# Optimization experiments

Measured on AMD Instinct MI355X. Metric: run time of the kernel, lower is better.

The kernel has to match this reference:

```python
import jax, jax.numpy as jnp
import numpy as np

B, N, H, NH, E = 4, 512, 1024, 16, 8
DH = H // NH  # head dim 64


def setup_inputs() -> dict:
    key = jax.random.key(0)
    ks = jax.random.split(key, 8)
    return {
        "hidden_states": jax.random.normal(ks[0], (B, N, H), jnp.float32),
        "attn_mask": jax.random.randint(ks[1], (N, N), 0, 2, jnp.int32),
        "key_padding_mask": jax.random.randint(ks[2], (B, N), 0, 2, jnp.int32),
        "w_gate": jax.random.normal(ks[3], (H, E), jnp.float32) * 0.02,
        "w_qkv": jax.random.normal(ks[4], (E, H, 3 * H), jnp.float32) * 0.02,
        "b_qkv": jnp.zeros((E, 3 * H), jnp.float32),
        "w_dense": jax.random.normal(ks[5], (E, H, H), jnp.float32) * 0.02,
        "b_dense": jnp.zeros((E, H), jnp.float32),
    }


def _moe_apply(x, combine, w, b):
    # x: [T,H], combine: [T,E] (one-hot * gate prob), w: [E,H,D], b: [E,D]
    out_all = jnp.einsum('th,ehd->etd', x, w) + b[:, None, :]  # [E,T,D]
    return jnp.einsum('te,etd->td', combine, out_all)


def reference(hidden_states, attn_mask, key_padding_mask, w_gate, w_qkv, b_qkv, w_dense, b_dense):
    b, n, h = hidden_states.shape
    # attention_mask = logical_or(attn_mask[None], key_padding_mask[:,None]) -> [B,N,N], then [:,None]*-1e4
    mask = jnp.logical_or(attn_mask[None].astype(bool), key_padding_mask[:, None].astype(bool))
    mask_bias = mask[:, None, :, :].astype(hidden_states.dtype) * (-10000.0)  # [B,1,N,N]

    x = hidden_states.reshape(-1, h)  # [T,H]
    gate = jax.nn.softmax(x @ w_gate, axis=-1)  # [T,E]
    # top-1 routing; combine weight = gate prob of chosen expert
    idx = jnp.argmax(gate, axis=-1)
    combine = jax.nn.one_hot(idx, gate.shape[-1], dtype=gate.dtype) * jnp.max(gate, axis=-1, keepdims=True)

    qkv = _moe_apply(x, combine, w_qkv, b_qkv).reshape(b, n, 3 * h)
    q, k, v = jnp.split(qkv, 3, axis=-1)
    # transpose_for_scores: [B,N,H] -> [B,NH,N,DH]
    to_heads = lambda t: t.reshape(b, n, NH, DH).transpose(0, 2, 1, 3)
    q, k, v = to_heads(q), to_heads(k), to_heads(v)

    scores = jnp.einsum('bhqd,bhkd->bhqk', q, k) / (float(DH) ** 0.5) + mask_bias
    attn_probs = jax.nn.softmax(scores, axis=-1)  # dropout p=0 -> identity
    ctx = jnp.einsum('bhqk,bhkd->bhqd', attn_probs, v)
    ctx = ctx.transpose(0, 2, 1, 3).reshape(-1, h)  # [T,H]

    out = _moe_apply(ctx, combine, w_dense, b_dense).reshape(b, n, h)
    return out, attn_probs
```

## Files before the change

### kernel.cpp

```cpp
#include <hip/hip_runtime.h>


typedef short short8 __attribute__((ext_vector_type(8)));
typedef float f32x4 __attribute__((ext_vector_type(4)));

constexpr int Bsz  = 4;
constexpr int Nseq = 512;
constexpr int Hdim = 1024;
constexpr int NHd  = 16;
constexpr int Ex   = 8;
constexpr int DHd  = 64;
constexpr int T    = Bsz * Nseq;
constexpr int H3   = 3 * Hdim;
constexpr int MAXT128 = 24;
constexpr int KB_N = 32;
constexpr int NPH  = KB_N / 2;

__device__ inline unsigned short f2bf(float f) {
  union { float f; unsigned u; } v{f};
  unsigned r = v.u + 0x7fffu + ((v.u >> 16) & 1u);
  return (unsigned short)(r >> 16);
}
__device__ inline float bf2f(unsigned short s) {
  union { unsigned u; float f; } v{(unsigned)s << 16};
  return v.f;
}
__device__ inline unsigned cvtpk2(float lo, float hi) {
  unsigned r;
  asm("v_cvt_pk_bf16_f32 %0, %1, %2" : "=v"(r) : "v"(lo), "v"(hi));
  return r;
}
__device__ inline void gl16(const unsigned short* g, unsigned short* l) {
  __builtin_amdgcn_global_load_lds(
      (const __attribute__((address_space(1))) unsigned int*)(g),
      (__attribute__((address_space(3))) unsigned int*)(l), 16, 0, 0);
}

__global__ __launch_bounds__(64) void gate_kernel(
    const float* __restrict__ x, const float* __restrict__ wg,
    float* __restrict__ prob, int* __restrict__ expert,
    unsigned short* __restrict__ Xb) {
  int t = blockIdx.x;
  int l = threadIdx.x;
  const float* xr = x + (size_t)t * Hdim;
  float acc[Ex] = {0, 0, 0, 0, 0, 0, 0, 0};
  for (int h = l; h < Hdim; h += 64) {
    float xv = xr[h];
    const float4* wr = (const float4*)(wg + (size_t)h * Ex);
    float4 w0 = wr[0], w1 = wr[1];
    acc[0] += xv * w0.x; acc[1] += xv * w0.y; acc[2] += xv * w0.z; acc[3] += xv * w0.w;
    acc[4] += xv * w1.x; acc[5] += xv * w1.y; acc[6] += xv * w1.z; acc[7] += xv * w1.w;
  }
  {
    const float4* s = (const float4*)(xr + l * 16);
    float4 f0 = s[0], f1 = s[1], f2 = s[2], f3 = s[3];
    unsigned q[8] = {cvtpk2(f0.x, f0.y), cvtpk2(f0.z, f0.w),
                     cvtpk2(f1.x, f1.y), cvtpk2(f1.z, f1.w),
                     cvtpk2(f2.x, f2.y), cvtpk2(f2.z, f2.w),
                     cvtpk2(f3.x, f3.y), cvtpk2(f3.z, f3.w)};
    uint4* d = (uint4*)(Xb + (size_t)t * Hdim + l * 16);
    d[0] = *(uint4*)&q[0];
    d[1] = *(uint4*)&q[4];
  }
#pragma unroll
  for (int e = 0; e < Ex; e++) {
#pragma unroll
    for (int off = 32; off > 0; off >>= 1) acc[e] += __shfl_down(acc[e], off);
  }
  if (l == 0) {
    float m = acc[0]; int mi = 0;
#pragma unroll
    for (int e = 1; e < Ex; e++) if (acc[e] > m) { m = acc[e]; mi = e; }
    float s = 0.f;
#pragma unroll
    for (int e = 0; e < Ex; e++) s += expf(acc[e] - m);
    prob[t]   = 1.0f / s;
    expert[t] = mi;
  }
}

__global__ __launch_bounds__(256) void prep_kernel(
    const float* __restrict__ Wq, const float* __restrict__ Wd,
    unsigned short* __restrict__ WtQ, unsigned short* __restrict__ WtD,
    const int* __restrict__ expert, int* offs, int* meta, int* te, int* tr,
    int* __restrict__ perm) {
  int bx = blockIdx.x, kb2 = blockIdx.y, e = blockIdx.z;
  int tid = threadIdx.x;

  if (bx == 32) {
    if (kb2 != 0 || e != 0) return;
    __shared__ int cnt[Ex];
    __shared__ int cur[Ex];
    if (tid < Ex) cnt[tid] = 0;
    __syncthreads();
    for (int t = tid; t < T; t += 256) atomicAdd(&cnt[expert[t]], 1);
    __syncthreads();
    if (tid == 0) {
      int o = 0, nt = 0;
      for (int ee = 0; ee < Ex; ee++) {
        offs[ee] = o; cur[ee] = o;
        int c = cnt[ee];
        for (int r = 0; r < c; r += 128) { te[nt] = ee; tr[nt] = o + r; nt++; }
        o += c;
      }
      offs[Ex] = o;
      meta[0] = nt;
    }
    __syncthreads();
    for (int t = tid; t < T; t += 256) {
      int slot = atomicAdd(&cur[expert[t]], 1);
      perm[slot] = t;
    }
    return;
  }

  const float* W;
  unsigned short* Wt;
  int ncb, NCOLS, NCB;
  if (bx < 24) { W = Wq; Wt = WtQ; ncb = bx;      NCOLS = H3;   NCB = 24; }
  else         { W = Wd; Wt = WtD; ncb = bx - 24; NCOLS = Hdim; NCB = 8;  }

  int c4 = tid & 31;
  int kg = (tid >> 5) & 3;
  int kh = tid >> 7;
  int kb = kb2 * 2 + kh;

  const float* src = W + ((size_t)e * Hdim + kb * 32 + kg * 8) * NCOLS + ncb * 128 + c4 * 4;
  float4 f[8];
#pragma unroll
  for (int j = 0; j < 8; j++) f[j] = *(const float4*)(src + (size_t)j * NCOLS);

  unsigned short* dst = Wt + (((size_t)e * NCB + ncb) * KB_N + kb) * 4096 +
                        (size_t)((c4 >> 2) * 64 + kg * 16 + (c4 & 3) * 4) * 8;
#pragma unroll
  for (int i = 0; i < 4; i++) {
    unsigned q[4] = {cvtpk2(f[0][i], f[1][i]), cvtpk2(f[2][i], f[3][i]),
                     cvtpk2(f[4][i], f[5][i]), cvtpk2(f[6][i], f[7][i])};
    *(uint4*)(dst + (size_t)i * 8) = *(uint4*)q;
  }
}

template <int BN>
__global__ __launch_bounds__(256) void moe_gemm_v13(
    const unsigned short* __restrict__ Xb, const unsigned short* __restrict__ Wt,
    const float* __restrict__ bias, const float* __restrict__ prob,
    const int* __restrict__ perm, const int* __restrict__ offs,
    const int* __restrict__ metap, const int* __restrict__ tile_e,
    const int* __restrict__ tile_r,
    unsigned short* __restrict__ Ybf, float* __restrict__ Yf, int Ncols) {
  constexpr int NF = BN / 32;
  int tIdx = blockIdx.y;
  if (tIdx >= metap[0]) return;
  int e = tile_e[tIdx], row0 = tile_r[tIdx];
  int rows = offs[e + 1] - row0; if (rows > 128) rows = 128;
  int col0 = blockIdx.x * BN;
  int ncb_n = Ncols >> 7;

  __shared__ unsigned short As[2 * 8192];
  __shared__ int   tok_s[128];
  __shared__ float p_s[128];

  int tid = threadIdx.x;
  if (tid < 128) {
    int rr = tid < rows ? tid : rows - 1;
    int tok = perm[row0 + rr];
    tok_s[tid] = tok; p_s[tid] = prob[tok];
  }
  __syncthreads();

  int lane = tid & 63, wave = tid >> 6;
  int l15 = lane & 15, l4 = lane >> 4;
  int wr = wave >> 1, wc = wave & 1;
  int aslotr = l4 ^ ((l15 >> 1) & 3);

  int arow0 = wave * 16 + (lane >> 2);
  int arow1 = arow0 + 64;
  int aslot0 = (lane & 3) ^ ((arow0 >> 1) & 3);
  int aslot1 = (lane & 3) ^ ((arow1 >> 1) & 3);
  const unsigned short* ag0 = Xb + (size_t)tok_s[arow0] * Hdim + aslot0 * 8;
  const unsigned short* ag1 = Xb + (size_t)tok_s[arow1] * Hdim + aslot1 * 8;

  const unsigned short* btile = Wt + (((size_t)e * ncb_n + (col0 >> 7)) * KB_N) * 4096;
  int Fb = ((col0 & 127) >> 4) + wc * NF;
  const unsigned short* bfrag = btile + ((size_t)(Fb * 64 + lane)) * 8;

  f32x4 acc[4][NF] = {};
  short8 bq[2][2][NF];

  gl16(ag0 + 0 * 32, As + 0 + wave * 512);
  gl16(ag1 + 0 * 32, As + 2048 + wave * 512);
  gl16(ag0 + 1 * 32, As + 4096 + wave * 512);
  gl16(ag1 + 1 * 32, As + 4096 + 2048 + wave * 512);
  asm volatile("" ::: "memory");
#pragma unroll
  for (int t = 0; t < 2; t++)
#pragma unroll
    for (int n = 0; n < NF; n++)
      bq[0][t][n] = *(const short8*)(bfrag + (size_t)t * 4096 + n * 512);
#pragma unroll
  for (int t = 0; t < 2; t++)
#pragma unroll
    for (int n = 0; n < NF; n++)
      bq[1][t][n] = *(const short8*)(bfrag + (size_t)(2 + t) * 4096 + n * 512);
  asm volatile("" ::: "memory");

#define PHASE(PH, PAR)                                                             \
  {                                                                                \
    int kap = ((PH) + 1 < NPH) ? (PH) + 1 : NPH - 1;      \
    int kbp = ((PH) + 2 < NPH) ? (PH) + 2 : NPH - 1;      \
    asm volatile("s_waitcnt vmcnt(4) lgkmcnt(0)" ::: "memory");                    \
    __builtin_amdgcn_s_barrier();                                                  \
    asm volatile("" ::: "memory");                                                 \
    unsigned short* dA = As + ((PAR) ^ 1) * 8192;                                  \
    gl16(ag0 + (size_t)(2 * kap) * 32, dA + wave * 512);                           \
    gl16(ag1 + (size_t)(2 * kap) * 32, dA + 2048 + wave * 512);                    \
    gl16(ag0 + (size_t)(2 * kap + 1) * 32, dA + 4096 + wave * 512);                \
    gl16(ag1 + (size_t)(2 * kap + 1) * 32, dA + 4096 + 2048 + wave * 512);         \
    asm volatile("" ::: "memory");                                                 \
    _Pragma("unroll")                                                              \
    for (int t = 0; t < 2; t++) {                                                  \
      const unsigned short* rb = As + (PAR) * 8192 + t * 4096;                     \
      short8 a[4];                                                                 \
      _Pragma("unroll")                                                            \
      for (int m = 0; m < 4; m++)                                                  \
        a[m] = *(const short8*)&rb[(wr * 64 + m * 16 + l15) * 32 + aslotr * 8];    \
      _Pragma("unroll")                                                            \
      for (int n = 0; n < NF; n++)                                                 \
        _Pragma("unroll")                                                          \
        for (int m = 0; m < 4; m++)                                                \
          acc[m][n] = __builtin_amdgcn_mfma_f32_16x16x32_bf16(                     \
              a[m], bq[PAR][t][n], acc[m][n], 0, 0, 0);                            \
    }                                                                              \
    _Pragma("unroll")                                                              \
    for (int t = 0; t < 2; t++)                                                    \
      _Pragma("unroll")                                                            \
      for (int n = 0; n < NF; n++)                                                 \
        bq[PAR][t][n] =                                                            \
            *(const short8*)(bfrag + (size_t)(2 * kbp + t) * 4096 + n * 512);      \
  }

  for (int ph = 0; ph < NPH; ph += 2) {
    PHASE(ph, 0);
    PHASE(ph + 1, 1);
  }
#undef PHASE
  asm volatile("s_waitcnt vmcnt(0)" ::: "memory");

#pragma unroll
  for (int n = 0; n < NF; n++) {
    int colg = col0 + wc * (NF * 16) + n * 16 + l15;
    float bv = bias[(size_t)e * Ncols + colg];
#pragma unroll
    for (int m = 0; m < 4; m++) {
#pragma unroll
      for (int r = 0; r < 4; r++) {
        int row = wr * 64 + m * 16 + l4 * 4 + r;
        if (row < rows) {
          int tok = tok_s[row];
          float o = (acc[m][n][r] + bv) * p_s[row];
          if (Ybf) Ybf[(size_t)tok * Ncols + colg] = f2bf(o);
          else     Yf [(size_t)tok * Ncols + colg] = o;
        }
      }
    }
  }
}

__global__ __launch_bounds__(256) void attn_kernel(
    const unsigned short* __restrict__ qkvb, const int* __restrict__ attn_mask,
    const int* __restrict__ kp_mask, float* __restrict__ probs_out,
    unsigned short* __restrict__ ctxb) {
  int qt = blockIdx.x, h = blockIdx.y, b = blockIdx.z;
  int tid = threadIdx.x;

  __shared__ unsigned short Qs[32 * 72];
  __shared__ unsigned short KV[2][64 * 72];
  __shared__ unsigned short S[32 * 520];
  __shared__ float invs[32];

  int lane = tid & 63, wave = tid >> 6;
  int l15 = lane & 15, l4 = lane >> 4;

  {
    int r = tid >> 3, c = (tid & 7) * 8;
    int t = b * Nseq + qt * 32 + r;
    uint4 v = *(const uint4*)(qkvb + (size_t)t * H3 + h * DHd + c);
    unsigned short* u = (unsigned short*)&v;
    unsigned short tmp[8];
#pragma unroll
    for (int j = 0; j < 8; j++) tmp[j] = f2bf(bf2f(u[j]) * 0.125f);
    *(uint4*)&Qs[r * 72 + c] = *(uint4*)tmp;
  }

  int kr0 = tid >> 3, kc0 = (tid & 7) * 8;
  int kr1 = kr0 + 32;
  const unsigned short* kbase = qkvb + (size_t)(b * Nseq) * H3 + Hdim + h * DHd + kc0;
  uint4 rc0 = *(const uint4*)(kbase + (size_t)kr0 * H3);
  uint4 rc1 = *(const uint4*)(kbase + (size_t)kr1 * H3);
  int cur = 0;
  for (int kt = 0; kt < 8; kt++) {
    int kn = (kt + 1 < 8) ? kt + 1 : 7;
    uint4 nn0 = *(const uint4*)(kbase + (size_t)(kn * 64 + kr0) * H3);
    uint4 nn1 = *(const uint4*)(kbase + (size_t)(kn * 64 + kr1) * H3);
    *(uint4*)&KV[cur][kr0 * 72 + kc0] = rc0;
    *(uint4*)&KV[cur][kr1 * 72 + kc0] = rc1;
    asm volatile("s_waitcnt lgkmcnt(0)" ::: "memory");
    __builtin_amdgcn_s_barrier();
    asm volatile("" ::: "memory");

    f32x4 acc[2] = {};
#pragma unroll
    for (int kk = 0; kk < 2; kk++) {
      short8 bfr = *(const short8*)&KV[cur][(wave * 16 + l15) * 72 + kk * 32 + l4 * 8];
#pragma unroll
      for (int m = 0; m < 2; m++) {
        short8 afr = *(const short8*)&Qs[(m * 16 + l15) * 72 + kk * 32 + l4 * 8];
        acc[m] = __builtin_amdgcn_mfma_f32_16x16x32_bf16(afr, bfr, acc[m], 0, 0, 0);
      }
    }
    int key = kt * 64 + wave * 16 + l15;
#pragma unroll
    for (int m = 0; m < 2; m++) {
#pragma unroll
      for (int r = 0; r < 4; r++) {
        int row = m * 16 + l4 * 4 + r;
        S[row * 520 + key] = f2bf(acc[m][r]);
      }
    }
    rc0 = nn0; rc1 = nn1; cur ^= 1;
  }
  __syncthreads();

  float inv;
  int sr = tid >> 3, sg = tid & 7;
  float sv[8][8];
  {
    unsigned short* Srow = &S[sr * 520];
    const int* amrow = attn_mask + (qt * 32 + sr) * Nseq;
    const int* kprow = kp_mask + b * Nseq;
    float m = -3.0e38f;
#pragma unroll
    for (int i = 0; i < 8; i++) {
      int cb = (sg + 8 * i) * 8;
      uint4 v = *(const uint4*)&Srow[cb];
      unsigned short* u = (unsigned short*)&v;
      int4 a0 = *(const int4*)(amrow + cb);
      int4 a1 = *(const int4*)(amrow + cb + 4);
      int4 k0 = *(const int4*)(kprow + cb);
      int4 k1 = *(const int4*)(kprow + cb + 4);
      sv[i][0] = bf2f(u[0]) + ((a0.x | k0.x) ? -10000.0f : 0.0f);
      sv[i][1] = bf2f(u[1]) + ((a0.y | k0.y) ? -10000.0f : 0.0f);
      sv[i][2] = bf2f(u[2]) + ((a0.z | k0.z) ? -10000.0f : 0.0f);
      sv[i][3] = bf2f(u[3]) + ((a0.w | k0.w) ? -10000.0f : 0.0f);
      sv[i][4] = bf2f(u[4]) + ((a1.x | k1.x) ? -10000.0f : 0.0f);
      sv[i][5] = bf2f(u[5]) + ((a1.y | k1.y) ? -10000.0f : 0.0f);
      sv[i][6] = bf2f(u[6]) + ((a1.z | k1.z) ? -10000.0f : 0.0f);
      sv[i][7] = bf2f(u[7]) + ((a1.w | k1.w) ? -10000.0f : 0.0f);
#pragma unroll
      for (int j = 0; j < 8; j++) m = fmaxf(m, sv[i][j]);
    }
#pragma unroll
    for (int off = 1; off < 8; off <<= 1) m = fmaxf(m, __shfl_xor(m, off));
    float sum = 0.f;
#pragma unroll
    for (int i = 0; i < 8; i++) {
      int cb = (sg + 8 * i) * 8;
      unsigned short t2[8];
#pragma unroll
      for (int j = 0; j < 8; j++) {
        float p = expf(sv[i][j] - m);
        sv[i][j] = p;
        t2[j] = f2bf(p);
        sum += p;
      }
      *(uint4*)&Srow[cb] = *(uint4*)t2;
    }
#pragma unroll
    for (int off = 1; off < 8; off <<= 1) sum += __shfl_xor(sum, off);
    inv = 1.0f / sum;
    if (sg == 0) invs[sr] = inv;
  }
  __syncthreads();

  int kpair = tid & 31, vc = (tid >> 5) * 8;
  const unsigned short* vbase = qkvb + (size_t)(b * Nseq) * H3 + 2 * Hdim + h * DHd + vc;
  uint4 pv0 = *(const uint4*)(vbase + (size_t)(kpair * 2) * H3);
  uint4 pv1 = *(const uint4*)(vbase + (size_t)(kpair * 2 + 1) * H3);

  {
    float* dst = probs_out + (((size_t)(b * NHd + h) * Nseq + qt * 32 + sr) * Nseq);
#pragma unroll
    for (int i = 0; i < 8; i++) {
      int cb = (sg + 8 * i) * 8;
      float4 o0 = {sv[i][0] * inv, sv[i][1] * inv, sv[i][2] * inv, sv[i][3] * inv};
      float4 o1 = {sv[i][4] * inv, sv[i][5] * inv, sv[i][6] * inv, sv[i][7] * inv};
      *(float4*)(dst + cb)     = o0;
      *(float4*)(dst + cb + 4) = o1;
    }
  }

  f32x4 acc2[2] = {};
  cur = 0;
  for (int kt = 0; kt < 8; kt++) {
    int kn = (kt + 1 < 8) ? kt + 1 : 7;
    uint4 nv0 = *(const uint4*)(vbase + (size_t)(kn * 64 + kpair * 2) * H3);
    uint4 nv1 = *(const uint4*)(vbase + (size_t)(kn * 64 + kpair * 2 + 1) * H3);
    unsigned* a0 = (unsigned*)&pv0;
    unsigned* a1 = (unsigned*)&pv1;
#pragma unroll
    for (int i = 0; i < 4; i++) {
      unsigned lo = (a0[i] & 0xffffu) | (a1[i] << 16);
      unsigned hi = (a0[i] >> 16) | (a1[i] & 0xffff0000u);
      *(unsigned*)&KV[cur][(vc + 2 * i    ) * 72 + 2 * kpair] = lo;
      *(unsigned*)&KV[cur][(vc + 2 * i + 1) * 72 + 2 * kpair] = hi;
    }
    asm volatile("s_waitcnt lgkmcnt(0)" ::: "memory");
    __builtin_amdgcn_s_barrier();
    asm volatile("" ::: "memory");
#pragma unroll
    for (int kk = 0; kk < 2; kk++) {
      short8 bfr = *(const short8*)&KV[cur][(wave * 16 + l15) * 72 + kk * 32 + l4 * 8];
#pragma unroll
      for (int m = 0; m < 2; m++) {
        short8 pfr = *(const short8*)&S[(m * 16 + l15) * 520 + kt * 64 + kk * 32 + l4 * 8];
        acc2[m] = __builtin_amdgcn_mfma_f32_16x16x32_bf16(pfr, bfr, acc2[m], 0, 0, 0);
      }
    }
    pv0 = nv0; pv1 = nv1; cur ^= 1;
  }
#pragma unroll
  for (int m = 0; m < 2; m++) {
#pragma unroll
    for (int r = 0; r < 4; r++) {
      int row = m * 16 + l4 * 4 + r;
      int tq = b * Nseq + qt * 32 + row;
      ctxb[(size_t)tq * Hdim + h * DHd + wave * 16 + l15] = f2bf(acc2[m][r] * invs[row]);
    }
  }
}

extern "C" void kernel_launch(void* const* d_in, const int* in_sizes, int n_in,
                              void* d_out, int out_size, void* d_ws, size_t ws_size,
                              hipStream_t stream) {
  const float* hidden   = (const float*)d_in[0];
  const int*   attn_m   = (const int*)d_in[1];
  const int*   kp_m     = (const int*)d_in[2];
  const float* w_gate   = (const float*)d_in[3];
  const float* w_qkv    = (const float*)d_in[4];
  const float* b_qkv    = (const float*)d_in[5];
  const float* w_dense  = (const float*)d_in[6];
  const float* b_dense  = (const float*)d_in[7];

  float* out       = (float*)d_out;
  float* probs_out = out + (size_t)T * Hdim;

  unsigned short* WtQ = (unsigned short*)probs_out;

  float*          prob = (float*)d_ws;
  unsigned short* Xb   = (unsigned short*)(prob + 2048);
  unsigned short* qkvb = Xb + (size_t)T * Hdim;
  unsigned short* ctxb = qkvb + (size_t)T * H3;
  unsigned short* WtD  = ctxb + (size_t)T * Hdim;
  int*   ip     = (int*)(WtD + (size_t)Ex * Hdim * Hdim);
  int*   expert = ip;
  int*   perm   = ip + T;
  int*   offs   = ip + 2 * T;
  int*   meta   = offs + 12;
  int*   te     = meta + 4;
  int*   tr     = te + MAXT128;

  gate_kernel<<<T, 64, 0, stream>>>(hidden, w_gate, prob, expert, Xb);
  prep_kernel<<<dim3(33, KB_N / 2, Ex), 256, 0, stream>>>(
      w_qkv, w_dense, WtQ, WtD, expert, offs, meta, te, tr, perm);
  moe_gemm_v13<64><<<dim3(H3 / 64, MAXT128), 256, 0, stream>>>(
      Xb, WtQ, b_qkv, prob, perm, offs, meta, te, tr, qkvb, nullptr, H3);
  attn_kernel<<<dim3(16, NHd, Bsz), 256, 0, stream>>>(qkvb, attn_m, kp_m, probs_out, ctxb);
  moe_gemm_v13<64><<<dim3(Hdim / 64, MAXT128), 256, 0, stream>>>(
      ctxb, WtD, b_dense, prob, perm, offs, meta, te, tr, nullptr, out, Hdim);
}
```

Measured before the change: 139.5 us.

## Fuse fp32-to-bf16 weight conversion into MoE GEMM, drop separate prep pass

```diff
diff --git a/kernel.cpp b/kernel.cpp
--- a/kernel.cpp
+++ b/kernel.cpp
@@ -79,70 +79,37 @@
   }
 }
 
-__global__ __launch_bounds__(256) void prep_kernel(
-    const float* __restrict__ Wq, const float* __restrict__ Wd,
-    unsigned short* __restrict__ WtQ, unsigned short* __restrict__ WtD,
+__global__ __launch_bounds__(256) void route_kernel(
     const int* __restrict__ expert, int* offs, int* meta, int* te, int* tr,
     int* __restrict__ perm) {
-  int bx = blockIdx.x, kb2 = blockIdx.y, e = blockIdx.z;
+  __shared__ int cnt[Ex];
+  __shared__ int cur[Ex];
   int tid = threadIdx.x;
-
-  if (bx == 32) {
-    if (kb2 != 0 || e != 0) return;
-    __shared__ int cnt[Ex];
-    __shared__ int cur[Ex];
-    if (tid < Ex) cnt[tid] = 0;
-    __syncthreads();
-    for (int t = tid; t < T; t += 256) atomicAdd(&cnt[expert[t]], 1);
-    __syncthreads();
-    if (tid == 0) {
-      int o = 0, nt = 0;
-      for (int ee = 0; ee < Ex; ee++) {
-        offs[ee] = o; cur[ee] = o;
-        int c = cnt[ee];
-        for (int r = 0; r < c; r += 128) { te[nt] = ee; tr[nt] = o + r; nt++; }
-        o += c;
-      }
-      offs[Ex] = o;
-      meta[0] = nt;
-    }
-    __syncthreads();
-    for (int t = tid; t < T; t += 256) {
-      int slot = atomicAdd(&cur[expert[t]], 1);
-      perm[slot] = t;
-    }
-    return;
-  }
-
-  const float* W;
-  unsigned short* Wt;
-  int ncb, NCOLS, NCB;
-  if (bx < 24) { W = Wq; Wt = WtQ; ncb = bx;      NCOLS = H3;   NCB = 24; }
-  else         { W = Wd; Wt = WtD; ncb = bx - 24; NCOLS = Hdim; NCB = 8;  }
-
-  int c4 = tid & 31;
-  int kg = (tid >> 5) & 3;
-  int kh = tid >> 7;
-  int kb = kb2 * 2 + kh;
-
-  const float* src = W + ((size_t)e * Hdim + kb * 32 + kg * 8) * NCOLS + ncb * 128 + c4 * 4;
-  float4 f[8];
-#pragma unroll
-  for (int j = 0; j < 8; j++) f[j] = *(const float4*)(src + (size_t)j * NCOLS);
-
-  unsigned short* dst = Wt + (((size_t)e * NCB + ncb) * KB_N + kb) * 4096 +
-                        (size_t)((c4 >> 2) * 64 + kg * 16 + (c4 & 3) * 4) * 8;
-#pragma unroll
-  for (int i = 0; i < 4; i++) {
-    unsigned q[4] = {cvtpk2(f[0][i], f[1][i]), cvtpk2(f[2][i], f[3][i]),
-                     cvtpk2(f[4][i], f[5][i]), cvtpk2(f[6][i], f[7][i])};
-    *(uint4*)(dst + (size_t)i * 8) = *(uint4*)q;
+  if (tid < Ex) cnt[tid] = 0;
+  __syncthreads();
+  for (int t = tid; t < T; t += 256) atomicAdd(&cnt[expert[t]], 1);
+  __syncthreads();
+  if (tid == 0) {
+    int o = 0, nt = 0;
+    for (int ee = 0; ee < Ex; ee++) {
+      offs[ee] = o; cur[ee] = o;
+      int c = cnt[ee];
+      for (int r = 0; r < c; r += 128) { te[nt] = ee; tr[nt] = o + r; nt++; }
+      o += c;
+    }
+    offs[Ex] = o;
+    meta[0] = nt;
+  }
+  __syncthreads();
+  for (int t = tid; t < T; t += 256) {
+    int slot = atomicAdd(&cur[expert[t]], 1);
+    perm[slot] = t;
   }
 }
 
 template <int BN>
-__global__ __launch_bounds__(256) void moe_gemm_v13(
-    const unsigned short* __restrict__ Xb, const unsigned short* __restrict__ Wt,
+__global__ __launch_bounds__(256) void moe_gemm_v16(
+    const unsigned short* __restrict__ Xb, const float* __restrict__ Wf,
     const float* __restrict__ bias, const float* __restrict__ prob,
     const int* __restrict__ perm, const int* __restrict__ offs,
     const int* __restrict__ metap, const int* __restrict__ tile_e,
@@ -154,7 +121,6 @@
   int e = tile_e[tIdx], row0 = tile_r[tIdx];
   int rows = offs[e + 1] - row0; if (rows > 128) rows = 128;
   int col0 = blockIdx.x * BN;
-  int ncb_n = Ncols >> 7;
 
   __shared__ unsigned short As[2 * 8192];
   __shared__ int   tok_s[128];
@@ -180,35 +146,42 @@
   const unsigned short* ag0 = Xb + (size_t)tok_s[arow0] * Hdim + aslot0 * 8;
   const unsigned short* ag1 = Xb + (size_t)tok_s[arow1] * Hdim + aslot1 * 8;
 
-  const unsigned short* btile = Wt + (((size_t)e * ncb_n + (col0 >> 7)) * KB_N) * 4096;
-  int Fb = ((col0 & 127) >> 4) + wc * NF;
-  const unsigned short* bfrag = btile + ((size_t)(Fb * 64 + lane)) * 8;
+  const float* bpe = Wf + (size_t)e * Hdim * Ncols;
+  int voff[NF];
+#pragma unroll
+  for (int n = 0; n < NF; n++)
+    voff[n] = (l4 * 8) * Ncols + col0 + wc * (NF * 16) + n * 16 + l15;
 
   f32x4 acc[4][NF] = {};
-  short8 bq[2][2][NF];
-
+  float bqf[2][2][NF][8];
+
+#define BLOAD(PAR, KT)                                                         \
+  {                                                                            \
+    _Pragma("unroll")                                                          \
+    for (int t = 0; t < 2; t++)                                                \
+      _Pragma("unroll")                                                        \
+      for (int n = 0; n < NF; n++)                                             \
+        _Pragma("unroll")                                                      \
+        for (int j = 0; j < 8; j++)                                            \
+          bqf[PAR][t][n][j] =                                                  \
+              bpe[(size_t)(((KT) + t) * 32 + j) * Ncols + voff[n]];            \
+  }
+
+  BLOAD(0, 0);
+  asm volatile("" ::: "memory");
   gl16(ag0 + 0 * 32, As + 0 + wave * 512);
   gl16(ag1 + 0 * 32, As + 2048 + wave * 512);
   gl16(ag0 + 1 * 32, As + 4096 + wave * 512);
   gl16(ag1 + 1 * 32, As + 4096 + 2048 + wave * 512);
   asm volatile("" ::: "memory");
-#pragma unroll
-  for (int t = 0; t < 2; t++)
-#pragma unroll
-    for (int n = 0; n < NF; n++)
-      bq[0][t][n] = *(const short8*)(bfrag + (size_t)t * 4096 + n * 512);
-#pragma unroll
-  for (int t = 0; t < 2; t++)
-#pragma unroll
-    for (int n = 0; n < NF; n++)
-      bq[1][t][n] = *(const short8*)(bfrag + (size_t)(2 + t) * 4096 + n * 512);
+  BLOAD(1, 2);
   asm volatile("" ::: "memory");
 
 #define PHASE(PH, PAR)                                                             \
   {                                                                                \
     int kap = ((PH) + 1 < NPH) ? (PH) + 1 : NPH - 1;      \
     int kbp = ((PH) + 2 < NPH) ? (PH) + 2 : NPH - 1;      \
-    asm volatile("s_waitcnt vmcnt(4) lgkmcnt(0)" ::: "memory");                    \
+    asm volatile("s_waitcnt vmcnt(32)" ::: "memory");                              \
     __builtin_amdgcn_s_barrier();                                                  \
     asm volatile("" ::: "memory");                                                 \
     unsigned short* dA = As + ((PAR) ^ 1) * 8192;                                  \
@@ -225,18 +198,19 @@
       for (int m = 0; m < 4; m++)                                                  \
         a[m] = *(const short8*)&rb[(wr * 64 + m * 16 + l15) * 32 + aslotr * 8];    \
       _Pragma("unroll")                                                            \
-      for (int n = 0; n < NF; n++)                                                 \
+      for (int n = 0; n < NF; n++) {                                               \
+        unsigned qb[4];                                                            \
+        _Pragma("unroll")                                                          \
+        for (int jj = 0; jj < 4; jj++)                                             \
+          qb[jj] = cvtpk2(bqf[PAR][t][n][2 * jj], bqf[PAR][t][n][2 * jj + 1]);     \
+        short8 bfr = *(short8*)qb;                                                 \
         _Pragma("unroll")                                                          \
         for (int m = 0; m < 4; m++)                                                \
           acc[m][n] = __builtin_amdgcn_mfma_f32_16x16x32_bf16(                     \
-              a[m], bq[PAR][t][n], acc[m][n], 0, 0, 0);                            \
+              a[m], bfr, acc[m][n], 0, 0, 0);                                      \
+      }                                                                            \
     }                                                                              \
-    _Pragma("unroll")                                                              \
-    for (int t = 0; t < 2; t++)                                                    \
-      _Pragma("unroll")                                                            \
-      for (int n = 0; n < NF; n++)                                                 \
-        bq[PAR][t][n] =                                                            \
-            *(const short8*)(bfrag + (size_t)(2 * kbp + t) * 4096 + n * 512);      \
+    BLOAD(PAR, 2 * kbp);                                                           \
   }
 
   for (int ph = 0; ph < NPH; ph += 2) {
@@ -244,6 +218,7 @@
     PHASE(ph + 1, 1);
   }
 #undef PHASE
+#undef BLOAD
   asm volatile("s_waitcnt vmcnt(0)" ::: "memory");
 
 #pragma unroll
@@ -454,14 +429,11 @@
   float* out       = (float*)d_out;
   float* probs_out = out + (size_t)T * Hdim;
 
-  unsigned short* WtQ = (unsigned short*)probs_out;
-
   float*          prob = (float*)d_ws;
   unsigned short* Xb   = (unsigned short*)(prob + 2048);
   unsigned short* qkvb = Xb + (size_t)T * Hdim;
   unsigned short* ctxb = qkvb + (size_t)T * H3;
-  unsigned short* WtD  = ctxb + (size_t)T * Hdim;
-  int*   ip     = (int*)(WtD + (size_t)Ex * Hdim * Hdim);
+  int*   ip     = (int*)(ctxb + (size_t)T * Hdim);
   int*   expert = ip;
   int*   perm   = ip + T;
   int*   offs   = ip + 2 * T;
@@ -470,11 +442,10 @@
   int*   tr     = te + MAXT128;
 
   gate_kernel<<<T, 64, 0, stream>>>(hidden, w_gate, prob, expert, Xb);
-  prep_kernel<<<dim3(33, KB_N / 2, Ex), 256, 0, stream>>>(
-      w_qkv, w_dense, WtQ, WtD, expert, offs, meta, te, tr, perm);
-  moe_gemm_v13<64><<<dim3(H3 / 64, MAXT128), 256, 0, stream>>>(
-      Xb, WtQ, b_qkv, prob, perm, offs, meta, te, tr, qkvb, nullptr, H3);
+  route_kernel<<<1, 256, 0, stream>>>(expert, offs, meta, te, tr, perm);
+  moe_gemm_v16<64><<<dim3(H3 / 64, MAXT128), 256, 0, stream>>>(
+      Xb, w_qkv, b_qkv, prob, perm, offs, meta, te, tr, qkvb, nullptr, H3);
   attn_kernel<<<dim3(16, NHd, Bsz), 256, 0, stream>>>(qkvb, attn_m, kp_m, probs_out, ctxb);
-  moe_gemm_v13<64><<<dim3(Hdim / 64, MAXT128), 256, 0, stream>>>(
-      ctxb, WtD, b_dense, prob, perm, offs, meta, te, tr, nullptr, out, Hdim);
-}
+  moe_gemm_v16<64><<<dim3(Hdim / 64, MAXT128), 256, 0, stream>>>(
+      ctxb, w_dense, b_dense, prob, perm, offs, meta, te, tr, nullptr, out, Hdim);
+}
```

Result: faster. 133.0 us (-4.7%).
